# Kernel optimization log

Hardware: AMD Instinct MI355X
Metric: run time of the kernel (lower is better)

## Reference

```python
import jax, jax.numpy as jnp
import numpy as np

N, D = 8192, 128

def setup_inputs() -> dict:
    key = jax.random.key(0)
    kq, kk, kv = jax.random.split(key, 3)
    query = jax.random.normal(kq, (N, D), dtype=jnp.float32)
    key_t = jax.random.normal(kk, (N, D), dtype=jnp.float32)
    value = jax.random.normal(kv, (N, D), dtype=jnp.float32)
    return {"query": query, "key": key_t, "value": value}

def reference(query, key, value):
    # FlashAttention-2 online softmax over blocks is mathematically exact
    # softmax attention: out = softmax(Q K^T / sqrt(d)) V, no mask.
    d = query.shape[-1]
    scale = 1.0 / jnp.sqrt(jnp.asarray(d, dtype=query.dtype))
    scores = jnp.einsum('qd,kd->qk', query, key) * scale  # [n, n]
    probs = jax.nn.softmax(scores, axis=-1)
    return jnp.einsum('qk,kd->qd', probs, value)  # [n, d]
```

## Files before the change

### kernel.cpp

```cpp
#include <hip/hip_runtime.h>
#include <hip/hip_bf16.h>

#define ATTN_N 8192
#define ATTN_D 128
#define TKEYS 32
#define NTILES (ATTN_N / TKEYS)
#define TILE_ELEMS (TKEYS * ATTN_D)
#define QROWS 256
#define SPLITK 16
#define KTPB (NTILES / SPLITK)
#define NBUF 4

typedef __bf16 bf16_t;
typedef bf16_t bf16x8 __attribute__((ext_vector_type(8)));
typedef float f32x4 __attribute__((ext_vector_type(4)));

#if __has_builtin(__builtin_amdgcn_exp2f)
#define EXP2(x) __builtin_amdgcn_exp2f(x)
#else
#define EXP2(x) __expf((x) * 0.6931471805599453f)
#endif

__device__ __forceinline__ void dma16(const bf16_t* g, bf16_t* l) {
  __builtin_amdgcn_global_load_lds(
      (const __attribute__((address_space(1))) void*)g,
      (__attribute__((address_space(3))) void*)l, 16, 0, 0);
}

__global__ void prep_kernel(const float* __restrict__ q,
                            const float* __restrict__ k,
                            const float* __restrict__ v,
                            bf16_t* __restrict__ qb,
                            bf16_t* __restrict__ kswz,
                            bf16_t* __restrict__ vtswz) {
  __shared__ bf16_t tile[64][72];
  const int bk = blockIdx.x;
  const int bd = blockIdx.y;
  const int t = threadIdx.x;
  const float sc = 0.12751744f;

  const int row_l = t >> 2;
  const int key = bk * 64 + row_l;

#pragma unroll
  for (int u = 0; u < 2; ++u) {
    const int j = bd * 8 + (t & 3) * 2 + u;
    const float4* qs = (const float4*)(q + (size_t)key * ATTN_D + j * 8);
    const float4* ks = (const float4*)(k + (size_t)key * ATTN_D + j * 8);
    float4 a0 = qs[0], a1 = qs[1];
    float4 b0 = ks[0], b1 = ks[1];
    bf16x8 qo, ko;
    qo[0] = (bf16_t)(a0.x * sc); qo[1] = (bf16_t)(a0.y * sc);
    qo[2] = (bf16_t)(a0.z * sc); qo[3] = (bf16_t)(a0.w * sc);
    qo[4] = (bf16_t)(a1.x * sc); qo[5] = (bf16_t)(a1.y * sc);
    qo[6] = (bf16_t)(a1.z * sc); qo[7] = (bf16_t)(a1.w * sc);
    ko[0] = (bf16_t)b0.x; ko[1] = (bf16_t)b0.y;
    ko[2] = (bf16_t)b0.z; ko[3] = (bf16_t)b0.w;
    ko[4] = (bf16_t)b1.x; ko[5] = (bf16_t)b1.y;
    ko[6] = (bf16_t)b1.z; ko[7] = (bf16_t)b1.w;
    *(bf16x8*)(qb + (size_t)key * ATTN_D + j * 8) = qo;
    *(bf16x8*)(kswz + (size_t)key * ATTN_D + ((j ^ (key & 15)) * 8)) = ko;
  }

  {
    const float* src = v + (size_t)key * ATTN_D + bd * 64 + (t & 3) * 16;
#pragma unroll
    for (int u = 0; u < 4; ++u) {
      float4 a = ((const float4*)src)[u];
      tile[row_l][(t & 3) * 16 + u * 4 + 0] = (bf16_t)a.x;
      tile[row_l][(t & 3) * 16 + u * 4 + 1] = (bf16_t)a.y;
      tile[row_l][(t & 3) * 16 + u * 4 + 2] = (bf16_t)a.z;
      tile[row_l][(t & 3) * 16 + u * 4 + 3] = (bf16_t)a.w;
    }
  }
  __syncthreads();
  {
    const int d_l = t >> 2;
    const int d = bd * 64 + d_l;
    const int cq = t & 3;
#pragma unroll
    for (int h = 0; h < 2; ++h) {
      bf16x8 o;
#pragma unroll
      for (int j = 0; j < 8; ++j) {
        const int kl_ = h * 32 + ((j & 4) << 2) + 4 * cq + (j & 3);
        o[j] = tile[kl_][d_l];
      }
      *(bf16x8*)(vtswz + (size_t)(2 * bk + h) * TILE_ELEMS + d * TKEYS +
                 ((cq ^ ((d >> 1) & 3)) * 8)) = o;
    }
  }
}

__global__ __launch_bounds__(512, 4) void flash_attn_kernel(
    const bf16_t* __restrict__ qb, const bf16_t* __restrict__ kswz,
    const bf16_t* __restrict__ vtswz, float* __restrict__ partO,
    float* __restrict__ partL) {
  __shared__ __align__(16) bf16_t KV[NBUF][2][TILE_ELEMS];

  const int t = threadIdx.x;
  const int w = t >> 6;
  const int lane = t & 63;
  const int quad = lane >> 4;
  const int col = lane & 15;
  const int blk = blockIdx.x;
  const int qg = blk >> 4;
  const int kh = blk & 15;
  const int q0 = qg * QROWS;
  const int ktbase = kh * KTPB;
  const int stg = (qg & 1) * 8;

#define ISSUE_TILE(itx)                                                       \
  {                                                                           \
    const int nt_ = ktbase + ((stg + (itx)) & (KTPB - 1));                    \
    const int nb_ = (itx) & (NBUF - 1);                                       \
    dma16(kswz + (size_t)nt_ * TILE_ELEMS + t * 8, &KV[nb_][0][t * 8]);       \
    dma16(vtswz + (size_t)nt_ * TILE_ELEMS + t * 8, &KV[nb_][1][t * 8]);      \
  }

  int offK[4][2], offV[8];
#pragma unroll
  for (int c = 0; c < 4; ++c)
#pragma unroll
    for (int ks = 0; ks < 2; ++ks)
      offK[c][ks] = (ks * 16 + col) * ATTN_D + (((c * 4 + quad) ^ col) * 8);
#pragma unroll
  for (int ds = 0; ds < 8; ++ds)
    offV[ds] = (ds * 16 + col) * TKEYS + ((quad ^ ((col >> 1) & 3)) * 8);

  bf16x8 aq[2][4];
#pragma unroll
  for (int qs = 0; qs < 2; ++qs) {
    const int row = q0 + w * 32 + qs * 16 + col;
#pragma unroll
    for (int c = 0; c < 4; ++c)
      aq[qs][c] = *(const bf16x8*)(qb + (size_t)row * ATTN_D + c * 32 + quad * 8);
  }

  f32x4 oacc[2][8];
#pragma unroll
  for (int qs = 0; qs < 2; ++qs)
#pragma unroll
    for (int i = 0; i < 8; ++i) oacc[qs][i] = (f32x4){0.f, 0.f, 0.f, 0.f};
  float l_part[2] = {0.f, 0.f};

#pragma unroll
  for (int pt = 0; pt < 3; ++pt) ISSUE_TILE(pt);
  asm volatile("s_waitcnt vmcnt(4)" ::: "memory");
  __builtin_amdgcn_s_barrier();

  for (int it = 0; it < KTPB; ++it) {
    const int buf = it & (NBUF - 1);
    if (it + 3 < KTPB) ISSUE_TILE(it + 3);
    const bf16_t* Kb = KV[buf][0];
    const bf16_t* Vb = KV[buf][1];

    f32x4 s[2][2];
#pragma unroll
    for (int ks = 0; ks < 2; ++ks)
#pragma unroll
      for (int qs = 0; qs < 2; ++qs) s[ks][qs] = (f32x4){0.f, 0.f, 0.f, 0.f};
    __builtin_amdgcn_s_setprio(1);
#pragma unroll
    for (int c = 0; c < 4; ++c) {
      bf16x8 k0 = *(const bf16x8*)(Kb + offK[c][0]);
      bf16x8 k1 = *(const bf16x8*)(Kb + offK[c][1]);
      s[0][0] = __builtin_amdgcn_mfma_f32_16x16x32_bf16(k0, aq[0][c], s[0][0], 0, 0, 0);
      s[0][1] = __builtin_amdgcn_mfma_f32_16x16x32_bf16(k0, aq[1][c], s[0][1], 0, 0, 0);
      s[1][0] = __builtin_amdgcn_mfma_f32_16x16x32_bf16(k1, aq[0][c], s[1][0], 0, 0, 0);
      s[1][1] = __builtin_amdgcn_mfma_f32_16x16x32_bf16(k1, aq[1][c], s[1][1], 0, 0, 0);
    }
    __builtin_amdgcn_s_setprio(0);

    bf16x8 ap[2];
#pragma unroll
    for (int qs = 0; qs < 2; ++qs) {
      float pa0 = EXP2(s[0][qs][0]), pa1 = EXP2(s[0][qs][1]);
      float pa2 = EXP2(s[0][qs][2]), pa3 = EXP2(s[0][qs][3]);
      float pb0 = EXP2(s[1][qs][0]), pb1 = EXP2(s[1][qs][1]);
      float pb2 = EXP2(s[1][qs][2]), pb3 = EXP2(s[1][qs][3]);
      l_part[qs] += (pa0 + pa1 + pa2 + pa3) + (pb0 + pb1 + pb2 + pb3);
      ap[qs][0] = (bf16_t)pa0; ap[qs][1] = (bf16_t)pa1;
      ap[qs][2] = (bf16_t)pa2; ap[qs][3] = (bf16_t)pa3;
      ap[qs][4] = (bf16_t)pb0; ap[qs][5] = (bf16_t)pb1;
      ap[qs][6] = (bf16_t)pb2; ap[qs][7] = (bf16_t)pb3;
    }

    __builtin_amdgcn_s_setprio(1);
#pragma unroll
    for (int ds = 0; ds < 8; ++ds) {
      bf16x8 bv = *(const bf16x8*)(Vb + offV[ds]);
      oacc[0][ds] = __builtin_amdgcn_mfma_f32_16x16x32_bf16(ap[0], bv, oacc[0][ds], 0, 0, 0);
      oacc[1][ds] = __builtin_amdgcn_mfma_f32_16x16x32_bf16(ap[1], bv, oacc[1][ds], 0, 0, 0);
    }
    __builtin_amdgcn_s_setprio(0);

    if (it + 3 < KTPB) {
      asm volatile("s_waitcnt vmcnt(4)" ::: "memory");
      __builtin_amdgcn_s_barrier();
    } else if (it + 2 < KTPB) {
      asm volatile("s_waitcnt vmcnt(2)" ::: "memory");
      __builtin_amdgcn_s_barrier();
    } else if (it + 1 < KTPB) {
      asm volatile("s_waitcnt vmcnt(0)" ::: "memory");
      __builtin_amdgcn_s_barrier();
    }
  }

#pragma unroll
  for (int qs = 0; qs < 2; ++qs) {
    float v = l_part[qs];
    v += __shfl_xor(v, 16, 64);
    v += __shfl_xor(v, 32, 64);
    if (quad == 0)
      partL[(size_t)blk * QROWS + w * 32 + qs * 16 + col] = v;
  }

  {
    float* dst = partO + ((size_t)blk * QROWS + w * 32) * ATTN_D;
#pragma unroll
    for (int qs = 0; qs < 2; ++qs)
#pragma unroll
      for (int ds = 0; ds < 8; ++ds)
#pragma unroll
        for (int r = 0; r < 4; ++r)
          dst[(qs * 16 + quad * 4 + r) * ATTN_D + ds * 16 + col] = oacc[qs][ds][r];
  }
#undef ISSUE_TILE
}

__global__ void merge_kernel(const float* __restrict__ partO,
                             const float* __restrict__ partL,
                             float* __restrict__ out) {
  const int idx = blockIdx.x * blockDim.x + threadIdx.x;
  const int row = idx >> 5;
  const int gi = row >> 8;
  const int rl = row & 255;
  const int li = rl * 32 + (idx & 31);
  float L = 0.f;
  float4 acc = {0.f, 0.f, 0.f, 0.f};
#pragma unroll
  for (int i = 0; i < 16; ++i) {
    const size_t b = (size_t)(16 * gi + i);
    L += partL[b * QROWS + rl];
    float4 a = ((const float4*)(partO + b * (QROWS * ATTN_D)))[li];
    acc.x += a.x; acc.y += a.y; acc.z += a.z; acc.w += a.w;
  }
  const float invL = 1.0f / L;
  float4 o;
  o.x = acc.x * invL; o.y = acc.y * invL;
  o.z = acc.z * invL; o.w = acc.w * invL;
  ((float4*)out)[idx] = o;
}

extern "C" void kernel_launch(void* const* d_in, const int* in_sizes, int n_in,
                              void* d_out, int out_size, void* d_ws, size_t ws_size,
                              hipStream_t stream) {
  const float* q = (const float*)d_in[0];
  const float* k = (const float*)d_in[1];
  const float* v = (const float*)d_in[2];
  float* out = (float*)d_out;

  bf16_t* qb = (bf16_t*)d_ws;
  bf16_t* kswz = qb + (size_t)ATTN_N * ATTN_D;
  bf16_t* vtswz = kswz + (size_t)ATTN_N * ATTN_D;
  float* partO = (float*)(vtswz + (size_t)ATTN_N * ATTN_D);
  float* partL = partO + (size_t)512 * QROWS * ATTN_D;

  prep_kernel<<<dim3(ATTN_N / 64, 2), 256, 0, stream>>>(q, k, v, qb, kswz, vtswz);
  flash_attn_kernel<<<512, 512, 0, stream>>>(qb, kswz, vtswz, partO, partL);
  merge_kernel<<<(ATTN_N * ATTN_D / 4) / 256, 256, 0, stream>>>(partO, partL, out);
}
```

Baseline: 128.5 us.

## Double key tile to 64 and halve split-K to 8 partitions

Raises the keys per tile from 32 to 64 and splits the key dimension into 8 partitions instead of 16. Each block now runs half as many loop iterations, so it pays for half as many barriers, and the partial-output traffic to the merge step is halved. This requires a new V transpose swizzle, doubled DMA issues per tile and adjusted vmcnt waits. In exchange, the grid drops to 256 blocks with launch bounds of 2, which may leave CUs underfilled, and the larger LDS footprint (128KB for 4 buffers) limits residency.

```diff
diff --git a/kernel.cpp b/kernel.cpp
--- a/kernel.cpp
+++ b/kernel.cpp
@@ -3,11 +3,11 @@
 
 #define ATTN_N 8192
 #define ATTN_D 128
-#define TKEYS 32
+#define TKEYS 64
 #define NTILES (ATTN_N / TKEYS)
 #define TILE_ELEMS (TKEYS * ATTN_D)
 #define QROWS 256
-#define SPLITK 16
+#define SPLITK 8
 #define KTPB (NTILES / SPLITK)
 #define NBUF 4
 
@@ -77,22 +77,24 @@
   {
     const int d_l = t >> 2;
     const int d = bd * 64 + d_l;
-    const int cq = t & 3;
-#pragma unroll
-    for (int h = 0; h < 2; ++h) {
+#pragma unroll
+    for (int u = 0; u < 2; ++u) {
+      const int cc = (t & 3) * 2 + u;
+      const int h = cc >> 2;
+      const int qd = cc & 3;
       bf16x8 o;
 #pragma unroll
       for (int j = 0; j < 8; ++j) {
-        const int kl_ = h * 32 + ((j & 4) << 2) + 4 * cq + (j & 3);
+        const int kl_ = h * 32 + ((j & 4) << 2) + 4 * qd + (j & 3);
         o[j] = tile[kl_][d_l];
       }
-      *(bf16x8*)(vtswz + (size_t)(2 * bk + h) * TILE_ELEMS + d * TKEYS +
-                 ((cq ^ ((d >> 1) & 3)) * 8)) = o;
-    }
-  }
-}
-
-__global__ __launch_bounds__(512, 4) void flash_attn_kernel(
+      *(bf16x8*)(vtswz + (size_t)bk * TILE_ELEMS + d * TKEYS +
+                 ((cc ^ (d & 7)) * 8)) = o;
+    }
+  }
+}
+
+__global__ __launch_bounds__(512, 2) void flash_attn_kernel(
     const bf16_t* __restrict__ qb, const bf16_t* __restrict__ kswz,
     const bf16_t* __restrict__ vtswz, float* __restrict__ partO,
     float* __restrict__ partL) {
@@ -104,29 +106,36 @@
   const int quad = lane >> 4;
   const int col = lane & 15;
   const int blk = blockIdx.x;
-  const int qg = blk >> 4;
-  const int kh = blk & 15;
+  const int qg = blk >> 3;
+  const int kh = blk & 7;
   const int q0 = qg * QROWS;
   const int ktbase = kh * KTPB;
-  const int stg = (qg & 1) * 8;
+  const int stg = (qg & 3) * 4;
 
 #define ISSUE_TILE(itx)                                                       \
   {                                                                           \
     const int nt_ = ktbase + ((stg + (itx)) & (KTPB - 1));                    \
     const int nb_ = (itx) & (NBUF - 1);                                       \
-    dma16(kswz + (size_t)nt_ * TILE_ELEMS + t * 8, &KV[nb_][0][t * 8]);       \
-    dma16(vtswz + (size_t)nt_ * TILE_ELEMS + t * 8, &KV[nb_][1][t * 8]);      \
-  }
-
-  int offK[4][2], offV[8];
+    _Pragma("unroll")                                                         \
+    for (int u = 0; u < 2; ++u) {                                             \
+      dma16(kswz + (size_t)nt_ * TILE_ELEMS + t * 8 + u * 4096,               \
+            &KV[nb_][0][t * 8 + u * 4096]);                                   \
+      dma16(vtswz + (size_t)nt_ * TILE_ELEMS + t * 8 + u * 4096,              \
+            &KV[nb_][1][t * 8 + u * 4096]);                                   \
+    }                                                                         \
+  }
+
+  int offK[4][4], offV[8][2];
 #pragma unroll
   for (int c = 0; c < 4; ++c)
 #pragma unroll
-    for (int ks = 0; ks < 2; ++ks)
+    for (int ks = 0; ks < 4; ++ks)
       offK[c][ks] = (ks * 16 + col) * ATTN_D + (((c * 4 + quad) ^ col) * 8);
 #pragma unroll
   for (int ds = 0; ds < 8; ++ds)
-    offV[ds] = (ds * 16 + col) * TKEYS + ((quad ^ ((col >> 1) & 3)) * 8);
+#pragma unroll
+    for (int h = 0; h < 2; ++h)
+      offV[ds][h] = (ds * 16 + col) * TKEYS + (((h * 4 + quad) ^ (col & 7)) * 8);
 
   bf16x8 aq[2][4];
 #pragma unroll
@@ -146,7 +155,7 @@
 
 #pragma unroll
   for (int pt = 0; pt < 3; ++pt) ISSUE_TILE(pt);
-  asm volatile("s_waitcnt vmcnt(4)" ::: "memory");
+  asm volatile("s_waitcnt vmcnt(8)" ::: "memory");
   __builtin_amdgcn_s_barrier();
 
   for (int it = 0; it < KTPB; ++it) {
@@ -155,51 +164,57 @@
     const bf16_t* Kb = KV[buf][0];
     const bf16_t* Vb = KV[buf][1];
 
-    f32x4 s[2][2];
-#pragma unroll
-    for (int ks = 0; ks < 2; ++ks)
+    f32x4 s[4][2];
+#pragma unroll
+    for (int ks = 0; ks < 4; ++ks)
 #pragma unroll
       for (int qs = 0; qs < 2; ++qs) s[ks][qs] = (f32x4){0.f, 0.f, 0.f, 0.f};
     __builtin_amdgcn_s_setprio(1);
 #pragma unroll
     for (int c = 0; c < 4; ++c) {
-      bf16x8 k0 = *(const bf16x8*)(Kb + offK[c][0]);
-      bf16x8 k1 = *(const bf16x8*)(Kb + offK[c][1]);
-      s[0][0] = __builtin_amdgcn_mfma_f32_16x16x32_bf16(k0, aq[0][c], s[0][0], 0, 0, 0);
-      s[0][1] = __builtin_amdgcn_mfma_f32_16x16x32_bf16(k0, aq[1][c], s[0][1], 0, 0, 0);
-      s[1][0] = __builtin_amdgcn_mfma_f32_16x16x32_bf16(k1, aq[0][c], s[1][0], 0, 0, 0);
-      s[1][1] = __builtin_amdgcn_mfma_f32_16x16x32_bf16(k1, aq[1][c], s[1][1], 0, 0, 0);
+#pragma unroll
+      for (int ks = 0; ks < 4; ++ks) {
+        bf16x8 kf = *(const bf16x8*)(Kb + offK[c][ks]);
+        s[ks][0] = __builtin_amdgcn_mfma_f32_16x16x32_bf16(kf, aq[0][c], s[ks][0], 0, 0, 0);
+        s[ks][1] = __builtin_amdgcn_mfma_f32_16x16x32_bf16(kf, aq[1][c], s[ks][1], 0, 0, 0);
+      }
     }
     __builtin_amdgcn_s_setprio(0);
 
-    bf16x8 ap[2];
+    bf16x8 ap[2][2];
 #pragma unroll
     for (int qs = 0; qs < 2; ++qs) {
-      float pa0 = EXP2(s[0][qs][0]), pa1 = EXP2(s[0][qs][1]);
-      float pa2 = EXP2(s[0][qs][2]), pa3 = EXP2(s[0][qs][3]);
-      float pb0 = EXP2(s[1][qs][0]), pb1 = EXP2(s[1][qs][1]);
-      float pb2 = EXP2(s[1][qs][2]), pb3 = EXP2(s[1][qs][3]);
-      l_part[qs] += (pa0 + pa1 + pa2 + pa3) + (pb0 + pb1 + pb2 + pb3);
-      ap[qs][0] = (bf16_t)pa0; ap[qs][1] = (bf16_t)pa1;
-      ap[qs][2] = (bf16_t)pa2; ap[qs][3] = (bf16_t)pa3;
-      ap[qs][4] = (bf16_t)pb0; ap[qs][5] = (bf16_t)pb1;
-      ap[qs][6] = (bf16_t)pb2; ap[qs][7] = (bf16_t)pb3;
+#pragma unroll
+      for (int h = 0; h < 2; ++h) {
+        float pa0 = EXP2(s[2 * h][qs][0]), pa1 = EXP2(s[2 * h][qs][1]);
+        float pa2 = EXP2(s[2 * h][qs][2]), pa3 = EXP2(s[2 * h][qs][3]);
+        float pb0 = EXP2(s[2 * h + 1][qs][0]), pb1 = EXP2(s[2 * h + 1][qs][1]);
+        float pb2 = EXP2(s[2 * h + 1][qs][2]), pb3 = EXP2(s[2 * h + 1][qs][3]);
+        l_part[qs] += (pa0 + pa1 + pa2 + pa3) + (pb0 + pb1 + pb2 + pb3);
+        ap[qs][h][0] = (bf16_t)pa0; ap[qs][h][1] = (bf16_t)pa1;
+        ap[qs][h][2] = (bf16_t)pa2; ap[qs][h][3] = (bf16_t)pa3;
+        ap[qs][h][4] = (bf16_t)pb0; ap[qs][h][5] = (bf16_t)pb1;
+        ap[qs][h][6] = (bf16_t)pb2; ap[qs][h][7] = (bf16_t)pb3;
+      }
     }
 
     __builtin_amdgcn_s_setprio(1);
 #pragma unroll
     for (int ds = 0; ds < 8; ++ds) {
-      bf16x8 bv = *(const bf16x8*)(Vb + offV[ds]);
-      oacc[0][ds] = __builtin_amdgcn_mfma_f32_16x16x32_bf16(ap[0], bv, oacc[0][ds], 0, 0, 0);
-      oacc[1][ds] = __builtin_amdgcn_mfma_f32_16x16x32_bf16(ap[1], bv, oacc[1][ds], 0, 0, 0);
+#pragma unroll
+      for (int h = 0; h < 2; ++h) {
+        bf16x8 bv = *(const bf16x8*)(Vb + offV[ds][h]);
+        oacc[0][ds] = __builtin_amdgcn_mfma_f32_16x16x32_bf16(ap[0][h], bv, oacc[0][ds], 0, 0, 0);
+        oacc[1][ds] = __builtin_amdgcn_mfma_f32_16x16x32_bf16(ap[1][h], bv, oacc[1][ds], 0, 0, 0);
+      }
     }
     __builtin_amdgcn_s_setprio(0);
 
     if (it + 3 < KTPB) {
-      asm volatile("s_waitcnt vmcnt(4)" ::: "memory");
+      asm volatile("s_waitcnt vmcnt(8)" ::: "memory");
       __builtin_amdgcn_s_barrier();
     } else if (it + 2 < KTPB) {
-      asm volatile("s_waitcnt vmcnt(2)" ::: "memory");
+      asm volatile("s_waitcnt vmcnt(4)" ::: "memory");
       __builtin_amdgcn_s_barrier();
     } else if (it + 1 < KTPB) {
       asm volatile("s_waitcnt vmcnt(0)" ::: "memory");
@@ -240,8 +255,8 @@
   float L = 0.f;
   float4 acc = {0.f, 0.f, 0.f, 0.f};
 #pragma unroll
-  for (int i = 0; i < 16; ++i) {
-    const size_t b = (size_t)(16 * gi + i);
+  for (int i = 0; i < 8; ++i) {
+    const size_t b = (size_t)(8 * gi + i);
     L += partL[b * QROWS + rl];
     float4 a = ((const float4*)(partO + b * (QROWS * ATTN_D)))[li];
     acc.x += a.x; acc.y += a.y; acc.z += a.z; acc.w += a.w;
@@ -265,9 +280,9 @@
   bf16_t* kswz = qb + (size_t)ATTN_N * ATTN_D;
   bf16_t* vtswz = kswz + (size_t)ATTN_N * ATTN_D;
   float* partO = (float*)(vtswz + (size_t)ATTN_N * ATTN_D);
-  float* partL = partO + (size_t)512 * QROWS * ATTN_D;
+  float* partL = partO + (size_t)256 * QROWS * ATTN_D;
 
   prep_kernel<<<dim3(ATTN_N / 64, 2), 256, 0, stream>>>(q, k, v, qb, kswz, vtswz);
-  flash_attn_kernel<<<512, 512, 0, stream>>>(qb, kswz, vtswz, partO, partL);
+  flash_attn_kernel<<<256, 512, 0, stream>>>(qb, kswz, vtswz, partO, partL);
   merge_kernel<<<(ATTN_N * ATTN_D / 4) / 256, 256, 0, stream>>>(partO, partL, out);
 }
```

Result: faster. 103.7 us (-19.3%).

## Halve split-K, batch tile prefetch in periods of four with one barrier

Applied to the files above, without the earlier changes.

Reduces split-K from 16 to 8, so 256 blocks each process 32 key tiles, and raises LDS buffering to 8 tiles. The per-tile wait and barrier become one wait and barrier per period of 4 tiles, with the next 4 tiles issued at the start of each period. V fragments are now loaded before the exp step. The aim is less barrier overhead and a smaller partial-output write and merge, at the cost of fewer blocks (256, about one per CU), doubled LDS use and lower occupancy.

```diff
diff --git a/kernel.cpp b/kernel.cpp
--- a/kernel.cpp
+++ b/kernel.cpp
@@ -7,9 +7,10 @@
 #define NTILES (ATTN_N / TKEYS)
 #define TILE_ELEMS (TKEYS * ATTN_D)
 #define QROWS 256
-#define SPLITK 16
+#define SPLITK 8
 #define KTPB (NTILES / SPLITK)
-#define NBUF 4
+#define NBUF 8
+#define PERIOD 4
 
 typedef __bf16 bf16_t;
 typedef bf16_t bf16x8 __attribute__((ext_vector_type(8)));
@@ -92,7 +93,7 @@
   }
 }
 
-__global__ __launch_bounds__(512, 4) void flash_attn_kernel(
+__global__ __launch_bounds__(512, 2) void flash_attn_kernel(
     const bf16_t* __restrict__ qb, const bf16_t* __restrict__ kswz,
     const bf16_t* __restrict__ vtswz, float* __restrict__ partO,
     float* __restrict__ partL) {
@@ -104,11 +105,11 @@
   const int quad = lane >> 4;
   const int col = lane & 15;
   const int blk = blockIdx.x;
-  const int qg = blk >> 4;
-  const int kh = blk & 15;
+  const int qg = blk >> 3;
+  const int kh = blk & 7;
   const int q0 = qg * QROWS;
   const int ktbase = kh * KTPB;
-  const int stg = (qg & 1) * 8;
+  const int stg = (qg & 3) * 8;
 
 #define ISSUE_TILE(itx)                                                       \
   {                                                                           \
@@ -145,66 +146,69 @@
   float l_part[2] = {0.f, 0.f};
 
 #pragma unroll
-  for (int pt = 0; pt < 3; ++pt) ISSUE_TILE(pt);
-  asm volatile("s_waitcnt vmcnt(4)" ::: "memory");
+  for (int pt = 0; pt < PERIOD; ++pt) ISSUE_TILE(pt);
+  asm volatile("s_waitcnt vmcnt(0)" ::: "memory");
   __builtin_amdgcn_s_barrier();
 
-  for (int it = 0; it < KTPB; ++it) {
-    const int buf = it & (NBUF - 1);
-    if (it + 3 < KTPB) ISSUE_TILE(it + 3);
-    const bf16_t* Kb = KV[buf][0];
-    const bf16_t* Vb = KV[buf][1];
-
-    f32x4 s[2][2];
-#pragma unroll
-    for (int ks = 0; ks < 2; ++ks)
-#pragma unroll
-      for (int qs = 0; qs < 2; ++qs) s[ks][qs] = (f32x4){0.f, 0.f, 0.f, 0.f};
-    __builtin_amdgcn_s_setprio(1);
-#pragma unroll
-    for (int c = 0; c < 4; ++c) {
-      bf16x8 k0 = *(const bf16x8*)(Kb + offK[c][0]);
-      bf16x8 k1 = *(const bf16x8*)(Kb + offK[c][1]);
-      s[0][0] = __builtin_amdgcn_mfma_f32_16x16x32_bf16(k0, aq[0][c], s[0][0], 0, 0, 0);
-      s[0][1] = __builtin_amdgcn_mfma_f32_16x16x32_bf16(k0, aq[1][c], s[0][1], 0, 0, 0);
-      s[1][0] = __builtin_amdgcn_mfma_f32_16x16x32_bf16(k1, aq[0][c], s[1][0], 0, 0, 0);
-      s[1][1] = __builtin_amdgcn_mfma_f32_16x16x32_bf16(k1, aq[1][c], s[1][1], 0, 0, 0);
-    }
-    __builtin_amdgcn_s_setprio(0);
-
-    bf16x8 ap[2];
-#pragma unroll
-    for (int qs = 0; qs < 2; ++qs) {
-      float pa0 = EXP2(s[0][qs][0]), pa1 = EXP2(s[0][qs][1]);
-      float pa2 = EXP2(s[0][qs][2]), pa3 = EXP2(s[0][qs][3]);
-      float pb0 = EXP2(s[1][qs][0]), pb1 = EXP2(s[1][qs][1]);
-      float pb2 = EXP2(s[1][qs][2]), pb3 = EXP2(s[1][qs][3]);
-      l_part[qs] += (pa0 + pa1 + pa2 + pa3) + (pb0 + pb1 + pb2 + pb3);
-      ap[qs][0] = (bf16_t)pa0; ap[qs][1] = (bf16_t)pa1;
-      ap[qs][2] = (bf16_t)pa2; ap[qs][3] = (bf16_t)pa3;
-      ap[qs][4] = (bf16_t)pb0; ap[qs][5] = (bf16_t)pb1;
-      ap[qs][6] = (bf16_t)pb2; ap[qs][7] = (bf16_t)pb3;
-    }
-
-    __builtin_amdgcn_s_setprio(1);
-#pragma unroll
-    for (int ds = 0; ds < 8; ++ds) {
-      bf16x8 bv = *(const bf16x8*)(Vb + offV[ds]);
-      oacc[0][ds] = __builtin_amdgcn_mfma_f32_16x16x32_bf16(ap[0], bv, oacc[0][ds], 0, 0, 0);
-      oacc[1][ds] = __builtin_amdgcn_mfma_f32_16x16x32_bf16(ap[1], bv, oacc[1][ds], 0, 0, 0);
-    }
-    __builtin_amdgcn_s_setprio(0);
-
-    if (it + 3 < KTPB) {
-      asm volatile("s_waitcnt vmcnt(4)" ::: "memory");
-      __builtin_amdgcn_s_barrier();
-    } else if (it + 2 < KTPB) {
-      asm volatile("s_waitcnt vmcnt(2)" ::: "memory");
-      __builtin_amdgcn_s_barrier();
-    } else if (it + 1 < KTPB) {
-      asm volatile("s_waitcnt vmcnt(0)" ::: "memory");
-      __builtin_amdgcn_s_barrier();
-    }
+  for (int p = 0; p < KTPB; p += PERIOD) {
+    if (p + PERIOD < KTPB) {
+#pragma unroll
+      for (int j = 0; j < PERIOD; ++j) ISSUE_TILE(p + PERIOD + j);
+    }
+
+#pragma unroll
+    for (int j = 0; j < PERIOD; ++j) {
+      const int it = p + j;
+      const bf16_t* Kb = KV[it & (NBUF - 1)][0];
+      const bf16_t* Vb = KV[it & (NBUF - 1)][1];
+
+      f32x4 s[2][2];
+#pragma unroll
+      for (int ks = 0; ks < 2; ++ks)
+#pragma unroll
+        for (int qs = 0; qs < 2; ++qs) s[ks][qs] = (f32x4){0.f, 0.f, 0.f, 0.f};
+      __builtin_amdgcn_s_setprio(1);
+#pragma unroll
+      for (int c = 0; c < 4; ++c) {
+        bf16x8 k0 = *(const bf16x8*)(Kb + offK[c][0]);
+        bf16x8 k1 = *(const bf16x8*)(Kb + offK[c][1]);
+        s[0][0] = __builtin_amdgcn_mfma_f32_16x16x32_bf16(k0, aq[0][c], s[0][0], 0, 0, 0);
+        s[0][1] = __builtin_amdgcn_mfma_f32_16x16x32_bf16(k0, aq[1][c], s[0][1], 0, 0, 0);
+        s[1][0] = __builtin_amdgcn_mfma_f32_16x16x32_bf16(k1, aq[0][c], s[1][0], 0, 0, 0);
+        s[1][1] = __builtin_amdgcn_mfma_f32_16x16x32_bf16(k1, aq[1][c], s[1][1], 0, 0, 0);
+      }
+      __builtin_amdgcn_s_setprio(0);
+
+      bf16x8 bv[8];
+#pragma unroll
+      for (int ds = 0; ds < 8; ++ds)
+        bv[ds] = *(const bf16x8*)(Vb + offV[ds]);
+
+      bf16x8 ap[2];
+#pragma unroll
+      for (int qs = 0; qs < 2; ++qs) {
+        float pa0 = EXP2(s[0][qs][0]), pa1 = EXP2(s[0][qs][1]);
+        float pa2 = EXP2(s[0][qs][2]), pa3 = EXP2(s[0][qs][3]);
+        float pb0 = EXP2(s[1][qs][0]), pb1 = EXP2(s[1][qs][1]);
+        float pb2 = EXP2(s[1][qs][2]), pb3 = EXP2(s[1][qs][3]);
+        l_part[qs] += (pa0 + pa1 + pa2 + pa3) + (pb0 + pb1 + pb2 + pb3);
+        ap[qs][0] = (bf16_t)pa0; ap[qs][1] = (bf16_t)pa1;
+        ap[qs][2] = (bf16_t)pa2; ap[qs][3] = (bf16_t)pa3;
+        ap[qs][4] = (bf16_t)pb0; ap[qs][5] = (bf16_t)pb1;
+        ap[qs][6] = (bf16_t)pb2; ap[qs][7] = (bf16_t)pb3;
+      }
+
+      __builtin_amdgcn_s_setprio(1);
+#pragma unroll
+      for (int ds = 0; ds < 8; ++ds) {
+        oacc[0][ds] = __builtin_amdgcn_mfma_f32_16x16x32_bf16(ap[0], bv[ds], oacc[0][ds], 0, 0, 0);
+        oacc[1][ds] = __builtin_amdgcn_mfma_f32_16x16x32_bf16(ap[1], bv[ds], oacc[1][ds], 0, 0, 0);
+      }
+      __builtin_amdgcn_s_setprio(0);
+    }
+
+    asm volatile("s_waitcnt vmcnt(0)" ::: "memory");
+    __builtin_amdgcn_s_barrier();
   }
 
 #pragma unroll
@@ -240,8 +244,8 @@
   float L = 0.f;
   float4 acc = {0.f, 0.f, 0.f, 0.f};
 #pragma unroll
-  for (int i = 0; i < 16; ++i) {
-    const size_t b = (size_t)(16 * gi + i);
+  for (int i = 0; i < 8; ++i) {
+    const size_t b = (size_t)(8 * gi + i);
     L += partL[b * QROWS + rl];
     float4 a = ((const float4*)(partO + b * (QROWS * ATTN_D)))[li];
     acc.x += a.x; acc.y += a.y; acc.z += a.z; acc.w += a.w;
@@ -265,9 +269,9 @@
   bf16_t* kswz = qb + (size_t)ATTN_N * ATTN_D;
   bf16_t* vtswz = kswz + (size_t)ATTN_N * ATTN_D;
   float* partO = (float*)(vtswz + (size_t)ATTN_N * ATTN_D);
-  float* partL = partO + (size_t)512 * QROWS * ATTN_D;
+  float* partL = partO + (size_t)256 * QROWS * ATTN_D;
 
   prep_kernel<<<dim3(ATTN_N / 64, 2), 256, 0, stream>>>(q, k, v, qb, kswz, vtswz);
-  flash_attn_kernel<<<512, 512, 0, stream>>>(qb, kswz, vtswz, partO, partL);
+  flash_attn_kernel<<<256, 512, 0, stream>>>(qb, kswz, vtswz, partO, partL);
   merge_kernel<<<(ATTN_N * ATTN_D / 4) / 256, 256, 0, stream>>>(partO, partL, out);
 }
```

Result: faster. 108.2 us (-15.8%).
